# Optimization experiments

Hardware: AMD Instinct MI355X
Metric: run time of the kernel (lower is better)

The kernel has to match this reference:

```python
import jax, jax.numpy as jnp
import numpy as np

DIM = 4096
N_HEADS = 32
N_KV_HEADS = 8
HEAD_DIM = DIM // N_HEADS  # 128
N_REP = N_HEADS // N_KV_HEADS  # 4
SEQ = 2048
BLOCK = 64
N_BLK = SEQ // BLOCK  # 32
TOPK = 8
NEG = -1e30


def _rope(x, cos, sin):
    # x: (B, L, H, D); cos/sin: (L, D/2). Pairs are interleaved (..., D/2, 2)
    B, L, H, D = x.shape
    xr = x.reshape(B, L, H, D // 2, 2)
    x0, x1 = xr[..., 0], xr[..., 1]
    c = cos[None, :, None, :]
    s = sin[None, :, None, :]
    o0 = x0 * c - x1 * s
    o1 = x0 * s + x1 * c
    return jnp.stack([o0, o1], axis=-1).reshape(B, L, H, D)


def setup_inputs() -> dict:
    key = jax.random.key(0)
    ks = jax.random.split(key, 8)
    x = jax.random.normal(ks[0], (1, SEQ, DIM), dtype=jnp.float32)
    # true RoPE angles (theta = 10000^{-2i/D})
    inv_freq = 1.0 / (10000.0 ** (np.arange(0, HEAD_DIM, 2, dtype=np.float32) / HEAD_DIM))
    angles = np.arange(SEQ, dtype=np.float32)[:, None] * inv_freq[None, :]  # (L, D/2)
    cos = jnp.asarray(np.cos(angles))
    sin = jnp.asarray(np.sin(angles))
    sc = 0.02
    wq = jax.random.normal(ks[1], (DIM, N_HEADS * HEAD_DIM), dtype=jnp.float32) * sc
    wk = jax.random.normal(ks[2], (DIM, N_KV_HEADS * HEAD_DIM), dtype=jnp.float32) * sc
    wv = jax.random.normal(ks[3], (DIM, N_KV_HEADS * HEAD_DIM), dtype=jnp.float32) * sc
    wo = jax.random.normal(ks[4], (N_HEADS * HEAD_DIM, DIM), dtype=jnp.float32) * sc
    return {"x": x, "cos": cos, "sin": sin, "wq": wq, "wk": wk, "wv": wv, "wo": wo}


def reference(x, cos, sin, wq, wk, wv, wo):
    B, L, _ = x.shape
    # QKV projections
    q = (x @ wq).reshape(B, L, N_HEADS, HEAD_DIM)
    k = (x @ wk).reshape(B, L, N_KV_HEADS, HEAD_DIM)
    v = (x @ wv).reshape(B, L, N_KV_HEADS, HEAD_DIM)
    # rotary embeddings on q and k
    q = _rope(q, cos, sin)
    k = _rope(k, cos, sin)
    # GQA: expand kv heads n_rep times
    k = jnp.repeat(k, N_REP, axis=2)  # (B, L, Hq, D)
    v = jnp.repeat(v, N_REP, axis=2)
    q = q.transpose(0, 2, 1, 3)  # (B, H, L, D)
    k = k.transpose(0, 2, 1, 3)
    v = v.transpose(0, 2, 1, 3)
    scale = 1.0 / jnp.sqrt(jnp.asarray(HEAD_DIM, dtype=q.dtype))

    pos = jnp.arange(L)
    causal = pos[None, :] <= pos[:, None]  # (Lq, Lk): key <= query

    # Block representatives: mean key per block -> top-k block selection per query
    k_blk = k.reshape(B, N_HEADS, N_BLK, BLOCK, HEAD_DIM).mean(axis=3)  # (B,H,Nblk,D)
    blk_scores = jnp.einsum('bhqd,bhnd->bhqn', q, k_blk) * scale  # (B,H,L,Nblk)
    blk_start = jnp.arange(N_BLK) * BLOCK
    blk_allowed = blk_start[None, :] <= pos[:, None]  # (L, Nblk)
    blk_scores = jnp.where(blk_allowed[None, None], blk_scores, NEG)
    _, top_idx = jax.lax.top_k(blk_scores, TOPK)  # (B,H,L,TOPK)
    blk_mask = jax.nn.one_hot(top_idx, N_BLK, dtype=jnp.bool_).any(axis=-2)  # (B,H,L,Nblk)

    # Expand block mask to per-key mask, combine with causal
    key_mask = jnp.repeat(blk_mask, BLOCK, axis=-1)  # (B,H,L,S)
    key_mask = key_mask & causal[None, None]

    scores = jnp.einsum('bhqd,bhkd->bhqk', q, k) * scale  # (B,H,L,S)
    scores = jnp.where(key_mask, scores, NEG)
    attn = jax.nn.softmax(scores, axis=-1)
    out = jnp.einsum('bhqk,bhkd->bhqd', attn, v)  # (B,H,L,D)
    out = out.transpose(0, 2, 1, 3).reshape(B, L, N_HEADS * HEAD_DIM)
    return out @ wo
```

## Files before the change

kernel.cpp:

```cpp
#include <hip/hip_runtime.h>
#include <hip/hip_bf16.h>
#include <math.h>

#define SEQ 2048
#define DIM 4096
#define NH 32
#define HD 128
#define NKV 8
#define NREP 4
#define BLOCK 64
#define NBLK 32
#define TOPK 8
#define KVDIM (NKV * HD)
#define SCALE 0.08838834764831845f

__device__ inline unsigned short f2b(float f) {
    __hip_bfloat16 h = __float2bfloat16(f);
    return *reinterpret_cast<unsigned short*>(&h);
}
__device__ inline float bitsf(unsigned int u) {
    union { float f; unsigned int i; } x; x.i = u; return x.f;
}
__device__ inline float b2f(unsigned short us) { return bitsf(((unsigned int)us) << 16); }
__device__ inline void unpack2(unsigned int w0, float* o) {
    o[0] = bitsf(w0 << 16);
    o[1] = bitsf(w0 & 0xffff0000u);
}
__device__ inline void unpack4(uint2 w, float* o) { unpack2(w.x, o); unpack2(w.y, o + 2); }
__device__ inline void unpack8(uint4 w, float* o) {
    unpack2(w.x, o); unpack2(w.y, o + 2); unpack2(w.z, o + 4); unpack2(w.w, o + 6);
}
__device__ inline float dot4f(float4 a, float4 b) {
    return a.x * b.x + a.y * b.y + a.z * b.z + a.w * b.w;
}

typedef __attribute__((ext_vector_type(8))) short bfrag;
typedef __attribute__((ext_vector_type(4))) float ffrag;

__device__ __forceinline__ void gl_lds16(const void* g, void* l) {
    __builtin_amdgcn_global_load_lds((const __attribute__((address_space(1))) void*)g,
                                     (__attribute__((address_space(3))) void*)l, 16, 0, 0);
}

template <bool SPLIT>
__global__ __launch_bounds__(256) void mfma_gemm(const unsigned short* __restrict__ Ah,
                                                 const unsigned short* __restrict__ Al,
                                                 const unsigned short* __restrict__ Bh,
                                                 const unsigned short* __restrict__ Bl,
                                                 float* __restrict__ C,
                                                 int M, int N, int K) {
    __shared__ short As[(SPLIT ? 2 : 1) * 4096];
    __shared__ short Bs[(SPLIT ? 2 : 1) * 4096];

    const int tid = threadIdx.x;
    const int lane = tid & 63;
    const int w = tid >> 6;
    const int wm = (w >> 1) * 64;
    const int wn = (w & 1) * 64;
    const int m = lane & 15;
    const int quad = lane >> 4;
    const int bm = blockIdx.y * 128;
    const int bn = blockIdx.x * 128;

    const int r0 = tid >> 2;
    const int c0 = (tid & 3) * 8;
    const size_t aoff0 = (size_t)(bm + r0) * K + c0;
    const size_t aoff1 = (size_t)(bm + r0 + 64) * K + c0;
    const size_t boff0 = (size_t)(bn + r0) * K + c0;
    const size_t boff1 = (size_t)(bn + r0 + 64) * K + c0;

    ffrag acc[4][4];
    const ffrag z = {0.f, 0.f, 0.f, 0.f};
#pragma unroll
    for (int i = 0; i < 4; ++i)
#pragma unroll
        for (int j = 0; j < 4; ++j) acc[i][j] = z;

    for (int kt = 0; kt < K; kt += 32) {
        __syncthreads();
        gl_lds16(Ah + aoff0 + kt, As + tid * 8);
        gl_lds16(Ah + aoff1 + kt, As + 2048 + tid * 8);
        gl_lds16(Bh + boff0 + kt, Bs + tid * 8);
        gl_lds16(Bh + boff1 + kt, Bs + 2048 + tid * 8);
        if constexpr (SPLIT) {
            gl_lds16(Al + aoff0 + kt, As + 4096 + tid * 8);
            gl_lds16(Al + aoff1 + kt, As + 6144 + tid * 8);
            gl_lds16(Bl + boff0 + kt, Bs + 4096 + tid * 8);
            gl_lds16(Bl + boff1 + kt, Bs + 6144 + tid * 8);
        }
        __syncthreads();

        bfrag ah[4], bh[4];
#pragma unroll
        for (int i = 0; i < 4; ++i)
            ah[i] = *(const bfrag*)(As + (wm + i * 16 + m) * 32 + quad * 8);
#pragma unroll
        for (int j = 0; j < 4; ++j)
            bh[j] = *(const bfrag*)(Bs + (wn + j * 16 + m) * 32 + quad * 8);
        if constexpr (SPLIT) {
            bfrag al[4], bl[4];
#pragma unroll
            for (int i = 0; i < 4; ++i)
                al[i] = *(const bfrag*)(As + 4096 + (wm + i * 16 + m) * 32 + quad * 8);
#pragma unroll
            for (int j = 0; j < 4; ++j)
                bl[j] = *(const bfrag*)(Bs + 4096 + (wn + j * 16 + m) * 32 + quad * 8);
#pragma unroll
            for (int i = 0; i < 4; ++i)
#pragma unroll
                for (int j = 0; j < 4; ++j) {
                    acc[i][j] = __builtin_amdgcn_mfma_f32_16x16x32_bf16(ah[i], bh[j], acc[i][j], 0, 0, 0);
                    acc[i][j] = __builtin_amdgcn_mfma_f32_16x16x32_bf16(ah[i], bl[j], acc[i][j], 0, 0, 0);
                    acc[i][j] = __builtin_amdgcn_mfma_f32_16x16x32_bf16(al[i], bh[j], acc[i][j], 0, 0, 0);
                }
        } else {
#pragma unroll
            for (int i = 0; i < 4; ++i)
#pragma unroll
                for (int j = 0; j < 4; ++j)
                    acc[i][j] = __builtin_amdgcn_mfma_f32_16x16x32_bf16(ah[i], bh[j], acc[i][j], 0, 0, 0);
        }
    }

#pragma unroll
    for (int i = 0; i < 4; ++i)
#pragma unroll
        for (int j = 0; j < 4; ++j)
#pragma unroll
            for (int r = 0; r < 4; ++r)
                C[(size_t)(bm + wm + i * 16 + quad * 4 + r) * N + bn + wn + j * 16 + m] =
                    acc[i][j][r];
}

__global__ __launch_bounds__(256) void transpose_conv(const float* __restrict__ W,
                                                      unsigned short* __restrict__ Th,
                                                      unsigned short* __restrict__ Tl,
                                                      int K, int N, int rowoff) {
    __shared__ float tile[32][36];
    const int k0 = blockIdx.y * 32, n0 = blockIdx.x * 32;
    const int t = threadIdx.x;
    const int r = t >> 3, c4 = (t & 7) * 4;
    *(float4*)&tile[r][c4] = *(const float4*)(W + (size_t)(k0 + r) * N + n0 + c4);
    __syncthreads();
    float v0 = tile[c4 + 0][r], v1 = tile[c4 + 1][r], v2 = tile[c4 + 2][r], v3 = tile[c4 + 3][r];
    ushort4 h;
    h.x = f2b(v0); h.y = f2b(v1); h.z = f2b(v2); h.w = f2b(v3);
    const size_t ooff = (size_t)(rowoff + n0 + r) * K + k0 + c4;
    *(ushort4*)(Th + ooff) = h;
    if (Tl) {
        ushort4 l;
        l.x = f2b(v0 - b2f(h.x)); l.y = f2b(v1 - b2f(h.y));
        l.z = f2b(v2 - b2f(h.z)); l.w = f2b(v3 - b2f(h.w));
        *(ushort4*)(Tl + ooff) = l;
    }
}

__global__ void conv_hilo(const float* __restrict__ X, unsigned short* __restrict__ H,
                          unsigned short* __restrict__ L) {
    const int i = (blockIdx.x * blockDim.x + threadIdx.x) * 4;
    const float4 x = *(const float4*)(X + i);
    ushort4 h;
    h.x = f2b(x.x); h.y = f2b(x.y); h.z = f2b(x.z); h.w = f2b(x.w);
    *(ushort4*)(H + i) = h;
    if (L) {
        ushort4 l;
        l.x = f2b(x.x - b2f(h.x)); l.y = f2b(x.y - b2f(h.y));
        l.z = f2b(x.z - b2f(h.z)); l.w = f2b(x.w - b2f(h.w));
        *(ushort4*)(L + i) = l;
    }
}

__global__ void kconv_kernel(const float* __restrict__ kvf, unsigned short* __restrict__ kb) {
    const int i = (blockIdx.x * blockDim.x + threadIdx.x) * 4;
    const int s = i >> 10, c = i & 1023;
    const float4 x = *(const float4*)(kvf + (size_t)s * 2048 + c);
    ushort4 h;
    h.x = f2b(x.x); h.y = f2b(x.y); h.z = f2b(x.z); h.w = f2b(x.w);
    *(ushort4*)(kb + (size_t)s * 1024 + c) = h;
}

__global__ __launch_bounds__(256) void vtrans_kernel(const float* __restrict__ kvf,
                                                     unsigned short* __restrict__ vt) {
    __shared__ unsigned short tile[64][72];
    const int s0 = blockIdx.x * 64;
    const int c0 = blockIdx.y * 64;
    const int t = threadIdx.x;
    const int r = t >> 4;
    const int c4 = (t & 15) * 4;
#pragma unroll
    for (int u = 0; u < 4; ++u) {
        const float4 x = *(const float4*)(kvf + (size_t)(s0 + u * 16 + r) * 2048 + 1024 + c0 + c4);
        ushort4 hh;
        hh.x = f2b(x.x); hh.y = f2b(x.y); hh.z = f2b(x.z); hh.w = f2b(x.w);
        *(ushort4*)(&tile[u * 16 + r][c4]) = hh;
    }
    __syncthreads();
    const int cc = t >> 2;
    const int sg = (t & 3) * 16;
    union { unsigned short s[16]; uint4 v[2]; } bb;
#pragma unroll
    for (int i = 0; i < 16; ++i) bb.s[i] = tile[sg + i][cc];
    unsigned short* op = vt + (size_t)(c0 + cc) * 2048 + s0 + sg;
    *(uint4*)op = bb.v[0];
    *(uint4*)(op + 8) = bb.v[1];
}

__global__ __launch_bounds__(256) void gemm_kernel(const float* __restrict__ A,
                                                   const float* __restrict__ B,
                                                   float* __restrict__ C,
                                                   int M, int N, int K) {
    __shared__ __align__(16) float As[16][68];
    __shared__ __align__(16) float Bs[16][68];

    const int tid = threadIdx.x;
    const int bm = blockIdx.y * 64;
    const int bn = blockIdx.x * 64;
    const int tm = (tid >> 4) * 4;
    const int tn = (tid & 15) * 4;

    float acc[4][4] = {};

    for (int k0 = 0; k0 < K; k0 += 16) {
        {
            const int mm = tid >> 2;
            const int kk = (tid & 3) * 4;
            const float* ap = A + (size_t)(bm + mm) * K + k0 + kk;
            const float4 a4 = *reinterpret_cast<const float4*>(ap);
            As[kk + 0][mm] = a4.x;
            As[kk + 1][mm] = a4.y;
            As[kk + 2][mm] = a4.z;
            As[kk + 3][mm] = a4.w;
        }
        {
            const int kk = tid >> 4;
            const int n = (tid & 15) * 4;
            const float* bp = B + (size_t)(k0 + kk) * N + bn + n;
            *reinterpret_cast<float4*>(&Bs[kk][n]) = *reinterpret_cast<const float4*>(bp);
        }
        __syncthreads();
#pragma unroll
        for (int kk = 0; kk < 16; ++kk) {
            const float4 a4 = *reinterpret_cast<const float4*>(&As[kk][tm]);
            const float4 b4 = *reinterpret_cast<const float4*>(&Bs[kk][tn]);
            const float av[4] = {a4.x, a4.y, a4.z, a4.w};
            const float bv[4] = {b4.x, b4.y, b4.z, b4.w};
#pragma unroll
            for (int i = 0; i < 4; ++i)
#pragma unroll
                for (int j = 0; j < 4; ++j) acc[i][j] += av[i] * bv[j];
        }
        __syncthreads();
    }
#pragma unroll
    for (int i = 0; i < 4; ++i)
#pragma unroll
        for (int j = 0; j < 4; ++j)
            C[(size_t)(bm + tm + i) * N + bn + tn + j] = acc[i][j];
}

__global__ void rope_kernel(float* __restrict__ x, const float* __restrict__ cosb,
                            const float* __restrict__ sinb, int nh, int stride) {
    const int idx = blockIdx.x * blockDim.x + threadIdx.x;
    const int i = idx & 63;
    const int h = (idx >> 6) % nh;
    const int pos = idx / (64 * nh);
    const float c = cosb[pos * 64 + i];
    const float s = sinb[pos * 64 + i];
    float* p = x + (size_t)pos * stride + h * HD + 2 * i;
    const float x0 = p[0], x1 = p[1];
    p[0] = x0 * c - x1 * s;
    p[1] = x0 * s + x1 * c;
}

__global__ void blkmean_kernel(const float* __restrict__ k, float* __restrict__ kblk,
                               int stride) {
    const int idx = blockIdx.x * blockDim.x + threadIdx.x;
    const int d = idx & 127;
    const int blk = (idx >> 7) & 31;
    const int kv = idx >> 12;
    float s = 0.f;
#pragma unroll 8
    for (int r = 0; r < BLOCK; ++r)
        s += k[(size_t)(blk * BLOCK + r) * stride + kv * HD + d];
    kblk[idx] = s * (1.f / 64.f);
}

__global__ __launch_bounds__(256) void attn_mfma_kernel(const float* __restrict__ q,
                                                        const unsigned short* __restrict__ kbp,
                                                        const unsigned short* __restrict__ vtp,
                                                        const float* __restrict__ kblk,
                                                        float* __restrict__ out) {
    __shared__ __align__(16) unsigned char smem[62720];
    unsigned short* qsb = (unsigned short*)smem;
    unsigned short* ksb = (unsigned short*)(smem + 17408);
    unsigned short* vsb = (unsigned short*)(smem + 34816);
    unsigned short* psb = (unsigned short*)(smem + 53248);
    unsigned int*  selm = (unsigned int*)(smem + 62464);
    float* qff = (float*)smem;
    float* kbf = (float*)(smem + 33792);
    float* bsc = (float*)(smem + 50688);

    const int qt = 31 - blockIdx.x;
    const int h = blockIdx.y;
    const int kv = h >> 2;
    const int qbase = qt * 64;
    const int tid = threadIdx.x;
    const int lane = tid & 63;
    const int w = tid >> 6;
    const int m = lane & 15;
    const int quad = lane >> 4;
    const int wm = w * 16;

#pragma unroll
    for (int u = 0; u < 8; ++u) {
        const int idx = u * 1024 + tid * 4;
        const int qi = idx >> 7, d = idx & 127;
        *(float4*)(qff + qi * 132 + d) =
            *(const float4*)(q + ((size_t)((qbase + qi) * NH + h)) * HD + d);
    }
#pragma unroll
    for (int u = 0; u < 4; ++u) {
        const int idx = u * 1024 + tid * 4;
        const int b = idx >> 7, d = idx & 127;
        *(float4*)(kbf + b * 132 + d) =
            *(const float4*)(kblk + ((size_t)(kv * NBLK + b)) * HD + d);
    }
    __syncthreads();

    {
        float acc[4][2] = {};
#pragma unroll 4
        for (int d = 0; d < 128; d += 4) {
            float4 qv[4], kb2[2];
#pragma unroll
            for (int i = 0; i < 4; ++i) qv[i] = *(float4*)(qff + (quad + 4 * w + 16 * i) * 132 + d);
#pragma unroll
            for (int j = 0; j < 2; ++j) kb2[j] = *(float4*)(kbf + (m + 16 * j) * 132 + d);
#pragma unroll
            for (int i = 0; i < 4; ++i)
#pragma unroll
                for (int j = 0; j < 2; ++j) acc[i][j] += dot4f(qv[i], kb2[j]);
        }
#pragma unroll
        for (int i = 0; i < 4; ++i)
#pragma unroll
            for (int j = 0; j < 2; ++j) {
                const int b = m + 16 * j;
                if (b <= qt) bsc[(quad + 4 * w + 16 * i) * 33 + b] = acc[i][j];
            }
    }
    __syncthreads();

    if (tid < 64) {
        const int ns = (qt + 1 < TOPK) ? qt + 1 : TOPK;
        unsigned int sel = 0;
        const float* br = bsc + tid * 33;
        for (int t2 = 0; t2 < ns; ++t2) {
            float best = -3.4e38f; int bi = 0;
            for (int b = 0; b <= qt; ++b)
                if (!((sel >> b) & 1u) && br[b] > best) { best = br[b]; bi = b; }
            sel |= 1u << bi;
        }
        selm[tid] = sel;
    }
    __syncthreads();

    unsigned int uni = 0;
    {
        float tmp[32];
#pragma unroll
        for (int u = 0; u < 8; ++u) {
            const int idx = u * 1024 + tid * 4;
            *(float4*)(tmp + u * 4) = *(float4*)(qff + (idx >> 7) * 132 + (idx & 127));
        }
        for (int i = 0; i < 64; ++i) uni |= selm[i];
        __syncthreads();
#pragma unroll
        for (int u = 0; u < 8; ++u) {
            const int idx = u * 1024 + tid * 4;
            const int qi = idx >> 7, d = idx & 127;
            ushort4 qu;
            qu.x = f2b(tmp[u * 4 + 0]); qu.y = f2b(tmp[u * 4 + 1]);
            qu.z = f2b(tmp[u * 4 + 2]); qu.w = f2b(tmp[u * 4 + 3]);
            *(ushort4*)(qsb + qi * 136 + d) = qu;
        }
    }

    unsigned int selr[4];
#pragma unroll
    for (int r = 0; r < 4; ++r) selr[r] = selm[wm + quad * 4 + r];

    float m_run[4], l_run[4];
#pragma unroll
    for (int r = 0; r < 4; ++r) { m_run[r] = -3.0e38f; l_run[r] = 0.f; }
    ffrag o[8];
    const ffrag z = {0.f, 0.f, 0.f, 0.f};
#pragma unroll
    for (int n = 0; n < 8; ++n) o[n] = z;

    unsigned short* psw = psb + w * (16 * 72);

    for (int b = 0; b <= qt; ++b) {
        if (!((uni >> b) & 1u)) continue;
        __syncthreads();
#pragma unroll
        for (int u = 0; u < 4; ++u) {
            const int idx = u * 256 + tid;
            const int r = idx >> 4, dseg = (idx & 15) * 8;
            *(uint4*)(ksb + r * 136 + dseg) =
                *(const uint4*)(kbp + (size_t)(b * 64 + r) * 1024 + kv * 128 + dseg);
        }
#pragma unroll
        for (int u = 0; u < 4; ++u) {
            const int idx = u * 256 + tid;
            const int d = idx >> 3, ks8 = (idx & 7) * 8;
            *(uint4*)(vsb + d * 72 + ks8) =
                *(const uint4*)(vtp + (size_t)(kv * 128 + d) * 2048 + b * 64 + ks8);
        }
        __syncthreads();

        ffrag s[4];
#pragma unroll
        for (int j = 0; j < 4; ++j) s[j] = z;
#pragma unroll
        for (int ks = 0; ks < 4; ++ks) {
            const bfrag aq = *(const bfrag*)(qsb + (wm + m) * 136 + ks * 32 + quad * 8);
#pragma unroll
            for (int j = 0; j < 4; ++j) {
                const bfrag bk = *(const bfrag*)(ksb + (j * 16 + m) * 136 + ks * 32 + quad * 8);
                s[j] = __builtin_amdgcn_mfma_f32_16x16x32_bf16(aq, bk, s[j], 0, 0, 0);
            }
        }

        const bool diag = (b == qt);
        float a_r[4];
#pragma unroll
        for (int r = 0; r < 4; ++r) {
            const int rloc = quad * 4 + r;
            const int rtile = wm + rloc;
            const bool selb = (selr[r] >> b) & 1u;
            float sv[4];
#pragma unroll
            for (int j = 0; j < 4; ++j) {
                const int col = j * 16 + m;
                const bool valid = selb && (!diag || col <= rtile);
                sv[j] = valid ? s[j][r] * SCALE : -3.0e38f;
            }
            float t = fmaxf(fmaxf(sv[0], sv[1]), fmaxf(sv[2], sv[3]));
            t = fmaxf(t, __shfl_xor(t, 1));
            t = fmaxf(t, __shfl_xor(t, 2));
            t = fmaxf(t, __shfl_xor(t, 4));
            t = fmaxf(t, __shfl_xor(t, 8));
            const float mo = m_run[r];
            const float mn = fmaxf(mo, t);
            a_r[r] = __expf(mo - mn);
            float sum = 0.f;
#pragma unroll
            for (int j = 0; j < 4; ++j) {
                const float p = (sv[j] > -1.0e30f) ? __expf(sv[j] - mn) : 0.f;
                psw[rloc * 72 + j * 16 + m] = f2b(p);
                sum += p;
            }
            sum += __shfl_xor(sum, 1);
            sum += __shfl_xor(sum, 2);
            sum += __shfl_xor(sum, 4);
            sum += __shfl_xor(sum, 8);
            l_run[r] = l_run[r] * a_r[r] + sum;
            m_run[r] = mn;
        }
#pragma unroll
        for (int n = 0; n < 8; ++n)
#pragma unroll
            for (int r = 0; r < 4; ++r) o[n][r] *= a_r[r];

#pragma unroll
        for (int ks = 0; ks < 2; ++ks) {
            const bfrag pa = *(const bfrag*)(psw + m * 72 + ks * 32 + quad * 8);
#pragma unroll
            for (int n = 0; n < 8; ++n) {
                const bfrag bv = *(const bfrag*)(vsb + (n * 16 + m) * 72 + ks * 32 + quad * 8);
                o[n] = __builtin_amdgcn_mfma_f32_16x16x32_bf16(pa, bv, o[n], 0, 0, 0);
            }
        }
    }

#pragma unroll
    for (int r = 0; r < 4; ++r) {
        const float inv = 1.f / l_run[r];
        float* op = out + ((size_t)((qbase + wm + quad * 4 + r) * NH + h)) * HD + m;
#pragma unroll
        for (int n = 0; n < 8; ++n) op[n * 16] = o[n][r] * inv;
    }
}

__global__ __launch_bounds__(256) void attn_tile_kernel(const float* __restrict__ q,
                                                        const float* __restrict__ kptr,
                                                        const float* __restrict__ vptr,
                                                        const float* __restrict__ kblk,
                                                        float* __restrict__ out,
                                                        int kvstride) {
    __shared__ __align__(16) unsigned char smem[62464];
    unsigned short* ksb = (unsigned short*)smem;
    unsigned short* vsb = (unsigned short*)(smem + 17408);
    unsigned short* psb = (unsigned short*)(smem + 34816);
    unsigned short* qsb = (unsigned short*)(smem + 43520);
    float* mrow = (float*)(smem + 60928);
    float* lrow = (float*)(smem + 61184);
    float* arow = (float*)(smem + 61440);
    float* mnew = (float*)(smem + 61696);
    unsigned int* selm = (unsigned int*)(smem + 61952);
    float* qf  = (float*)smem;
    float* kbf = (float*)(smem + 33792);
    float* bsc = (float*)(smem + 50688);

    const int qt = 31 - blockIdx.x;
    const int h = blockIdx.y;
    const int kv = h >> 2;
    const int qbase = qt * 64;
    const int tid = threadIdx.x;
    const int lane = tid & 63;
    const int w = tid >> 6;
    const int kl = lane & 15;
    const int ql = lane >> 4;

#pragma unroll
    for (int u = 0; u < 8; ++u) {
        const int idx = u * 1024 + tid * 4;
        const int qi = idx >> 7, d = idx & 127;
        *(float4*)(qf + qi * 132 + d) =
            *(const float4*)(q + ((size_t)((qbase + qi) * NH + h)) * HD + d);
    }
#pragma unroll
    for (int u = 0; u < 4; ++u) {
        const int idx = u * 1024 + tid * 4;
        const int b = idx >> 7, d = idx & 127;
        *(float4*)(kbf + b * 132 + d) =
            *(const float4*)(kblk + ((size_t)(kv * NBLK + b)) * HD + d);
    }
    __syncthreads();

    {
        float acc[4][2] = {};
#pragma unroll 4
        for (int d = 0; d < 128; d += 4) {
            float4 qv[4], kb2[2];
#pragma unroll
            for (int i = 0; i < 4; ++i) qv[i] = *(float4*)(qf + (ql + 4 * w + 16 * i) * 132 + d);
#pragma unroll
            for (int j = 0; j < 2; ++j) kb2[j] = *(float4*)(kbf + (kl + 16 * j) * 132 + d);
#pragma unroll
            for (int i = 0; i < 4; ++i)
#pragma unroll
                for (int j = 0; j < 2; ++j) acc[i][j] += dot4f(qv[i], kb2[j]);
        }
#pragma unroll
        for (int i = 0; i < 4; ++i)
#pragma unroll
            for (int j = 0; j < 2; ++j) {
                const int b = kl + 16 * j;
                if (b <= qt) bsc[(ql + 4 * w + 16 * i) * 33 + b] = acc[i][j];
            }
    }
    __syncthreads();

    if (tid < 64) {
        const int ns = (qt + 1 < TOPK) ? qt + 1 : TOPK;
        unsigned int sel = 0;
        const float* br = bsc + tid * 33;
        for (int t = 0; t < ns; ++t) {
            float best = -3.4e38f; int bi = 0;
            for (int b = 0; b <= qt; ++b)
                if (!((sel >> b) & 1u) && br[b] > best) { best = br[b]; bi = b; }
            sel |= 1u << bi;
        }
        selm[tid] = sel;
        mrow[tid] = -3.0e38f;
        lrow[tid] = 0.f;
    }
    __syncthreads();

    unsigned int uni = 0;
    {
        float tmp[32];
#pragma unroll
        for (int u = 0; u < 8; ++u) {
            const int idx = u * 1024 + tid * 4;
            *(float4*)(tmp + u * 4) = *(float4*)(qf + (idx >> 7) * 132 + (idx & 127));
        }
        for (int i = 0; i < 64; ++i) uni |= selm[i];
#pragma unroll
        for (int u = 0; u < 8; ++u) {
            const int idx = u * 1024 + tid * 4;
            const int qi = idx >> 7, d = idx & 127;
            ushort4 qu;
            qu.x = f2b(tmp[u * 4 + 0]); qu.y = f2b(tmp[u * 4 + 1]);
            qu.z = f2b(tmp[u * 4 + 2]); qu.w = f2b(tmp[u * 4 + 3]);
            *(ushort4*)(qsb + qi * 136 + d) = qu;
        }
    }
    __syncthreads();

    const int qi_r[4] = {ql + 4 * w, ql + 4 * w + 16, ql + 4 * w + 32, ql + 4 * w + 48};
    unsigned int selq[4];
#pragma unroll
    for (int i = 0; i < 4; ++i) selq[i] = selm[qi_r[i]];

    float O[4][8] = {};

    for (int b = 0; b <= qt; ++b) {
        if (!((uni >> b) & 1u)) continue;
        __syncthreads();
#pragma unroll
        for (int u = 0; u < 8; ++u) {
            const int idx = u * 1024 + tid * 4;
            const int r = idx >> 7, d = idx & 127;
            const size_t gof = (size_t)(b * 64 + r) * kvstride + kv * HD + d;
            const float4 k4 = *(const float4*)(kptr + gof);
            const float4 v4 = *(const float4*)(vptr + gof);
            ushort4 ku, vu;
            ku.x = f2b(k4.x); ku.y = f2b(k4.y); ku.z = f2b(k4.z); ku.w = f2b(k4.w);
            vu.x = f2b(v4.x); vu.y = f2b(v4.y); vu.z = f2b(v4.z); vu.w = f2b(v4.w);
            *(ushort4*)(ksb + r * 136 + d) = ku;
            *(ushort4*)(vsb + r * 136 + d) = vu;
        }
        __syncthreads();

        float S[4][4] = {};
#pragma unroll 4
        for (int d = 0; d < 128; d += 4) {
            float qv[4][4], kk4[4][4];
#pragma unroll
            for (int i = 0; i < 4; ++i) unpack4(*(uint2*)(qsb + qi_r[i] * 136 + d), qv[i]);
#pragma unroll
            for (int j = 0; j < 4; ++j) unpack4(*(uint2*)(ksb + (kl + 16 * j) * 136 + d), kk4[j]);
#pragma unroll
            for (int i = 0; i < 4; ++i)
#pragma unroll
                for (int j = 0; j < 4; ++j)
#pragma unroll
                    for (int e = 0; e < 4; ++e) S[i][j] += qv[i][e] * kk4[j][e];
        }

        const bool diag = (b == qt);
        float tm[4];
#pragma unroll
        for (int i = 0; i < 4; ++i) {
            const bool selb = (selq[i] >> b) & 1u;
#pragma unroll
            for (int j = 0; j < 4; ++j) {
                const int kj = kl + 16 * j;
                const bool valid = selb && (!diag || kj <= qi_r[i]);
                S[i][j] = valid ? S[i][j] * SCALE : -3.0e38f;
            }
            float t = fmaxf(fmaxf(S[i][0], S[i][1]), fmaxf(S[i][2], S[i][3]));
            t = fmaxf(t, __shfl_xor(t, 1));
            t = fmaxf(t, __shfl_xor(t, 2));
            t = fmaxf(t, __shfl_xor(t, 4));
            t = fmaxf(t, __shfl_xor(t, 8));
            tm[i] = t;
        }
        if (kl == 0) {
#pragma unroll
            for (int i = 0; i < 4; ++i) {
                const float mo = mrow[qi_r[i]];
                const float mn = fmaxf(mo, tm[i]);
                mrow[qi_r[i]] = mn;
                mnew[qi_r[i]] = mn;
                arow[qi_r[i]] = __expf(mo - mn);
            }
        }
        __syncthreads();

        float tl[4];
#pragma unroll
        for (int i = 0; i < 4; ++i) {
            const float mn = mnew[qi_r[i]];
            float sum = 0.f;
#pragma unroll
            for (int j = 0; j < 4; ++j) {
                const float p = (S[i][j] > -1.0e30f) ? __expf(S[i][j] - mn) : 0.f;
                psb[qi_r[i] * 68 + kl + 16 * j] = f2b(p);
                sum += p;
            }
            sum += __shfl_xor(sum, 1);
            sum += __shfl_xor(sum, 2);
            sum += __shfl_xor(sum, 4);
            sum += __shfl_xor(sum, 8);
            tl[i] = sum;
        }
        if (kl == 0) {
#pragma unroll
            for (int i = 0; i < 4; ++i)
                lrow[qi_r[i]] = lrow[qi_r[i]] * arow[qi_r[i]] + tl[i];
        }
#pragma unroll
        for (int i = 0; i < 4; ++i) {
            const float a = arow[qi_r[i]];
#pragma unroll
            for (int e = 0; e < 8; ++e) O[i][e] *= a;
        }
        __syncthreads();

#pragma unroll 4
        for (int kj = 0; kj < 64; ++kj) {
            float p[4];
#pragma unroll
            for (int i = 0; i < 4; ++i) {
                unsigned short us = psb[qi_r[i] * 68 + kj];
                p[i] = bitsf(((unsigned int)us) << 16);
            }
            float vv[8];
            unpack8(*(uint4*)(vsb + kj * 136 + kl * 8), vv);
#pragma unroll
            for (int i = 0; i < 4; ++i)
#pragma unroll
                for (int e = 0; e < 8; ++e) O[i][e] += p[i] * vv[e];
        }
    }
    __syncthreads();

#pragma unroll
    for (int i = 0; i < 4; ++i) {
        const float inv = 1.f / lrow[qi_r[i]];
        float4 o0, o1;
        o0.x = O[i][0] * inv; o0.y = O[i][1] * inv; o0.z = O[i][2] * inv; o0.w = O[i][3] * inv;
        o1.x = O[i][4] * inv; o1.y = O[i][5] * inv; o1.z = O[i][6] * inv; o1.w = O[i][7] * inv;
        float* op = out + ((size_t)((qbase + qi_r[i]) * NH + h)) * HD + kl * 8;
        *(float4*)op = o0;
        *(float4*)(op + 4) = o1;
    }
}

extern "C" void kernel_launch(void* const* d_in, const int* in_sizes, int n_in,
                              void* d_out, int out_size, void* d_ws, size_t ws_size,
                              hipStream_t stream) {
    const float* x    = (const float*)d_in[0];
    const float* cosb = (const float*)d_in[1];
    const float* sinb = (const float*)d_in[2];
    const float* wq   = (const float*)d_in[3];
    const float* wk   = (const float*)d_in[4];
    const float* wv   = (const float*)d_in[5];
    const float* wo   = (const float*)d_in[6];

    unsigned char* ws = (unsigned char*)d_ws;
    const dim3 t256(256);

    const size_t MAIN_REQ = 184680448ull;
    if (ws_size >= MAIN_REQ) {
        float*          qf     = (float*)(ws);
        float*          kvf    = (float*)(ws + 33554432ull);
        float*          kblk   = (float*)(ws + 50331648ull);
        unsigned short* x_hi   = (unsigned short*)(ws + 50462720ull);
        unsigned short* x_lo   = (unsigned short*)(ws + 67239936ull);
        float*          attn   = (float*)(ws + 50462720ull);
        unsigned short* wqT_hi = (unsigned short*)(ws + 84017152ull);
        unsigned short* wqT_lo = (unsigned short*)(ws + 117571584ull);
        unsigned short* kvT_hi = (unsigned short*)(ws + 151126016ull);
        unsigned short* kvT_lo = (unsigned short*)(ws + 167903232ull);
        unsigned short* woT_hi = wqT_hi;
        unsigned short* attnbf = wqT_lo;
        unsigned short* kb16   = kvT_hi;
        unsigned short* vtb    = kvT_lo;

        conv_hilo<<<SEQ * DIM / 4 / 256, t256, 0, stream>>>(x, x_hi, x_lo);
        transpose_conv<<<dim3(DIM / 32, DIM / 32), t256, 0, stream>>>(wq, wqT_hi, wqT_lo, DIM, DIM, 0);
        transpose_conv<<<dim3(KVDIM / 32, DIM / 32), t256, 0, stream>>>(wk, kvT_hi, kvT_lo, DIM, KVDIM, 0);
        transpose_conv<<<dim3(KVDIM / 32, DIM / 32), t256, 0, stream>>>(wv, kvT_hi, kvT_lo, DIM, KVDIM, KVDIM);

        hipLaunchKernelGGL((mfma_gemm<true>), dim3(DIM / 128, SEQ / 128), t256, 0, stream,
                           x_hi, x_lo, wqT_hi, wqT_lo, qf, SEQ, DIM, DIM);
        hipLaunchKernelGGL((mfma_gemm<true>), dim3(2 * KVDIM / 128, SEQ / 128), t256, 0, stream,
                           x_hi, x_lo, kvT_hi, kvT_lo, kvf, SEQ, 2 * KVDIM, DIM);
        transpose_conv<<<dim3(DIM / 32, DIM / 32), t256, 0, stream>>>(wo, woT_hi, nullptr, DIM, DIM, 0);

        rope_kernel<<<(SEQ * NH * 64) / 256, t256, 0, stream>>>(qf, cosb, sinb, NH, NH * HD);
        rope_kernel<<<(SEQ * NKV * 64) / 256, t256, 0, stream>>>(kvf, cosb, sinb, NKV, 2 * KVDIM);
        blkmean_kernel<<<(NKV * NBLK * HD) / 256, t256, 0, stream>>>(kvf, kblk, 2 * KVDIM);

        kconv_kernel<<<(SEQ * KVDIM / 4) / 256, t256, 0, stream>>>(kvf, kb16);
        vtrans_kernel<<<dim3(SEQ / 64, KVDIM / 64), t256, 0, stream>>>(kvf, vtb);

        attn_mfma_kernel<<<dim3(NBLK, NH), t256, 0, stream>>>(qf, kb16, vtb, kblk, attn);

        conv_hilo<<<SEQ * DIM / 4 / 256, t256, 0, stream>>>(attn, attnbf, nullptr);
        hipLaunchKernelGGL((mfma_gemm<false>), dim3(DIM / 128, SEQ / 128), t256, 0, stream,
                           attnbf, nullptr, woT_hi, nullptr, (float*)d_out, SEQ, DIM, DIM);
    } else {
        float* qf   = (float*)ws;
        float* kf   = qf + (size_t)SEQ * DIM;
        float* vf   = kf + (size_t)SEQ * KVDIM;
        float* kblk = vf + (size_t)SEQ * KVDIM;
        float* attn = kblk + (size_t)NKV * NBLK * HD;

        gemm_kernel<<<dim3(DIM / 64, SEQ / 64), t256, 0, stream>>>(x, wq, qf, SEQ, DIM, DIM);
        gemm_kernel<<<dim3(KVDIM / 64, SEQ / 64), t256, 0, stream>>>(x, wk, kf, SEQ, KVDIM, DIM);
        gemm_kernel<<<dim3(KVDIM / 64, SEQ / 64), t256, 0, stream>>>(x, wv, vf, SEQ, KVDIM, DIM);
        rope_kernel<<<(SEQ * NH * 64) / 256, t256, 0, stream>>>(qf, cosb, sinb, NH, NH * HD);
        rope_kernel<<<(SEQ * NKV * 64) / 256, t256, 0, stream>>>(kf, cosb, sinb, NKV, KVDIM);
        blkmean_kernel<<<(NKV * NBLK * HD) / 256, t256, 0, stream>>>(kf, kblk, KVDIM);
        attn_tile_kernel<<<dim3(NBLK, NH), t256, 0, stream>>>(qf, kf, vf, kblk, attn, KVDIM);
        gemm_kernel<<<dim3(DIM / 64, SEQ / 64), t256, 0, stream>>>(attn, wo, (float*)d_out, SEQ, DIM, DIM);
    }
}
```

Before: 940.8 us.

## Prefetch K/V tiles into registers, keep Q in registers, skip top-k for early tiles

The attention kernel now keeps the Q fragments in registers as bf16 and no longer stages Q in shared memory. This shrinks LDS use so three workgroups can fit per CU. It iterates only over the selected blocks via ctz and prefetches the next K/V tile into registers while the current one is computed. Block scoring and top-k are skipped when the query tile has at most TOPK causal blocks, since all of them are selected anyway. It also adds MFMA priority hints and an XCD-aware workgroup swizzle in both the GEMM and the attention kernel. The cost is higher register pressure from the prefetch buffers.

```diff
diff --git a/kernel.cpp b/kernel.cpp
--- a/kernel.cpp
+++ b/kernel.cpp
@@ -59,8 +59,20 @@
     const int wn = (w & 1) * 64;
     const int m = lane & 15;
     const int quad = lane >> 4;
-    const int bm = blockIdx.y * 128;
-    const int bn = blockIdx.x * 128;
+
+    int bx = blockIdx.x, by = blockIdx.y;
+    {
+        const int nwg = gridDim.x * gridDim.y;
+        if ((nwg & 7) == 0) {
+            const int flat = by * gridDim.x + bx;
+            const int nper = nwg >> 3;
+            const int swz = (flat & 7) * nper + (flat >> 3);
+            bx = swz % gridDim.x;
+            by = swz / gridDim.x;
+        }
+    }
+    const int bm = by * 128;
+    const int bn = bx * 128;
 
     const int r0 = tid >> 2;
     const int c0 = (tid & 3) * 8;
@@ -285,23 +297,28 @@
     kblk[idx] = s * (1.f / 64.f);
 }
 
-__global__ __launch_bounds__(256) void attn_mfma_kernel(const float* __restrict__ q,
-                                                        const unsigned short* __restrict__ kbp,
-                                                        const unsigned short* __restrict__ vtp,
-                                                        const float* __restrict__ kblk,
-                                                        float* __restrict__ out) {
-    __shared__ __align__(16) unsigned char smem[62720];
-    unsigned short* qsb = (unsigned short*)smem;
-    unsigned short* ksb = (unsigned short*)(smem + 17408);
-    unsigned short* vsb = (unsigned short*)(smem + 34816);
-    unsigned short* psb = (unsigned short*)(smem + 53248);
-    unsigned int*  selm = (unsigned int*)(smem + 62464);
-    float* qff = (float*)smem;
-    float* kbf = (float*)(smem + 33792);
-    float* bsc = (float*)(smem + 50688);
-
-    const int qt = 31 - blockIdx.x;
-    const int h = blockIdx.y;
+__global__ __launch_bounds__(256, 3) void attn_mfma_kernel(const float* __restrict__ q,
+                                                           const unsigned short* __restrict__ kbp,
+                                                           const unsigned short* __restrict__ vtp,
+                                                           const float* __restrict__ kblk,
+                                                           float* __restrict__ out) {
+    __shared__ __align__(16) unsigned char smem[45568];
+    unsigned short* ksb = (unsigned short*)smem;
+    unsigned short* vsb = (unsigned short*)(smem + 17408);
+    unsigned short* psb = (unsigned short*)(smem + 35840);
+    unsigned int*  selm = (unsigned int*)(smem + 45056);
+    float* kbf = (float*)smem;
+    float* bsc = (float*)(smem + 16896);
+
+    int bx = blockIdx.x, by = blockIdx.y;
+    {
+        const int flat = by * 32 + bx;
+        const int swz = (flat & 7) * 128 + (flat >> 3);
+        bx = swz & 31;
+        by = swz >> 5;
+    }
+    const int qt = 31 - bx;
+    const int h = by;
     const int kv = h >> 2;
     const int qbase = qt * 64;
     const int tid = threadIdx.x;
@@ -311,84 +328,80 @@
     const int quad = lane >> 4;
     const int wm = w * 16;
 
-#pragma unroll
-    for (int u = 0; u < 8; ++u) {
-        const int idx = u * 1024 + tid * 4;
-        const int qi = idx >> 7, d = idx & 127;
-        *(float4*)(qff + qi * 132 + d) =
-            *(const float4*)(q + ((size_t)((qbase + qi) * NH + h)) * HD + d);
-    }
-#pragma unroll
-    for (int u = 0; u < 4; ++u) {
-        const int idx = u * 1024 + tid * 4;
-        const int b = idx >> 7, d = idx & 127;
-        *(float4*)(kbf + b * 132 + d) =
-            *(const float4*)(kblk + ((size_t)(kv * NBLK + b)) * HD + d);
-    }
-    __syncthreads();
-
+    unsigned int uni;
+    if (qt + 1 > TOPK) {
+#pragma unroll
+        for (int u = 0; u < 4; ++u) {
+            const int idx = u * 1024 + tid * 4;
+            const int b = idx >> 7, d = idx & 127;
+            *(float4*)(kbf + b * 132 + d) =
+                *(const float4*)(kblk + ((size_t)(kv * NBLK + b)) * HD + d);
+        }
+        __syncthreads();
+        {
+            float acc[4][2] = {};
+            const int r0 = quad + 4 * w;
+#pragma unroll 4
+            for (int d = 0; d < 128; d += 4) {
+                float4 qv[4], kb2[2];
+#pragma unroll
+                for (int i = 0; i < 4; ++i)
+                    qv[i] = *(const float4*)(q + ((size_t)((qbase + r0 + 16 * i) * NH + h)) * HD + d);
+#pragma unroll
+                for (int j = 0; j < 2; ++j) kb2[j] = *(float4*)(kbf + (m + 16 * j) * 132 + d);
+#pragma unroll
+                for (int i = 0; i < 4; ++i)
+#pragma unroll
+                    for (int j = 0; j < 2; ++j) acc[i][j] += dot4f(qv[i], kb2[j]);
+            }
+#pragma unroll
+            for (int i = 0; i < 4; ++i)
+#pragma unroll
+                for (int j = 0; j < 2; ++j) {
+                    const int b = m + 16 * j;
+                    if (b <= qt) bsc[(r0 + 16 * i) * 33 + b] = acc[i][j];
+                }
+        }
+        __syncthreads();
+        if (tid < 64) {
+            unsigned int sel = 0;
+            const float* br = bsc + tid * 33;
+            for (int t2 = 0; t2 < TOPK; ++t2) {
+                float best = -3.4e38f; int bi = 0;
+                for (int b = 0; b <= qt; ++b)
+                    if (!((sel >> b) & 1u) && br[b] > best) { best = br[b]; bi = b; }
+                sel |= 1u << bi;
+            }
+            selm[tid] = sel;
+        }
+        __syncthreads();
+        unsigned int u2 = 0;
+        for (int i = 0; i < 64; ++i) u2 |= selm[i];
+        uni = u2;
+    } else {
+        uni = (2u << qt) - 1;
+    }
+
+    unsigned int selr[4];
+#pragma unroll
+    for (int r = 0; r < 4; ++r)
+        selr[r] = (qt + 1 > TOPK) ? selm[wm + quad * 4 + r] : uni;
+
+    bfrag aq[4];
     {
-        float acc[4][2] = {};
-#pragma unroll 4
-        for (int d = 0; d < 128; d += 4) {
-            float4 qv[4], kb2[2];
-#pragma unroll
-            for (int i = 0; i < 4; ++i) qv[i] = *(float4*)(qff + (quad + 4 * w + 16 * i) * 132 + d);
-#pragma unroll
-            for (int j = 0; j < 2; ++j) kb2[j] = *(float4*)(kbf + (m + 16 * j) * 132 + d);
-#pragma unroll
-            for (int i = 0; i < 4; ++i)
-#pragma unroll
-                for (int j = 0; j < 2; ++j) acc[i][j] += dot4f(qv[i], kb2[j]);
-        }
-#pragma unroll
-        for (int i = 0; i < 4; ++i)
-#pragma unroll
-            for (int j = 0; j < 2; ++j) {
-                const int b = m + 16 * j;
-                if (b <= qt) bsc[(quad + 4 * w + 16 * i) * 33 + b] = acc[i][j];
-            }
-    }
-    __syncthreads();
-
-    if (tid < 64) {
-        const int ns = (qt + 1 < TOPK) ? qt + 1 : TOPK;
-        unsigned int sel = 0;
-        const float* br = bsc + tid * 33;
-        for (int t2 = 0; t2 < ns; ++t2) {
-            float best = -3.4e38f; int bi = 0;
-            for (int b = 0; b <= qt; ++b)
-                if (!((sel >> b) & 1u) && br[b] > best) { best = br[b]; bi = b; }
-            sel |= 1u << bi;
-        }
-        selm[tid] = sel;
-    }
-    __syncthreads();
-
-    unsigned int uni = 0;
-    {
-        float tmp[32];
-#pragma unroll
-        for (int u = 0; u < 8; ++u) {
-            const int idx = u * 1024 + tid * 4;
-            *(float4*)(tmp + u * 4) = *(float4*)(qff + (idx >> 7) * 132 + (idx & 127));
-        }
-        for (int i = 0; i < 64; ++i) uni |= selm[i];
-        __syncthreads();
-#pragma unroll
-        for (int u = 0; u < 8; ++u) {
-            const int idx = u * 1024 + tid * 4;
-            const int qi = idx >> 7, d = idx & 127;
-            ushort4 qu;
-            qu.x = f2b(tmp[u * 4 + 0]); qu.y = f2b(tmp[u * 4 + 1]);
-            qu.z = f2b(tmp[u * 4 + 2]); qu.w = f2b(tmp[u * 4 + 3]);
-            *(ushort4*)(qsb + qi * 136 + d) = qu;
-        }
-    }
-
-    unsigned int selr[4];
-#pragma unroll
-    for (int r = 0; r < 4; ++r) selr[r] = selm[wm + quad * 4 + r];
+        const float* qrow = q + ((size_t)((qbase + wm + m) * NH + h)) * HD;
+#pragma unroll
+        for (int ks = 0; ks < 4; ++ks) {
+            const float4 f0 = *(const float4*)(qrow + ks * 32 + quad * 8);
+            const float4 f1 = *(const float4*)(qrow + ks * 32 + quad * 8 + 4);
+            bfrag a;
+            a[0] = (short)f2b(f0.x); a[1] = (short)f2b(f0.y);
+            a[2] = (short)f2b(f0.z); a[3] = (short)f2b(f0.w);
+            a[4] = (short)f2b(f1.x); a[5] = (short)f2b(f1.y);
+            a[6] = (short)f2b(f1.z); a[7] = (short)f2b(f1.w);
+            aq[ks] = a;
+        }
+    }
 
     float m_run[4], l_run[4];
 #pragma unroll
@@ -400,37 +413,65 @@
 
     unsigned short* psw = psb + w * (16 * 72);
 
-    for (int b = 0; b <= qt; ++b) {
-        if (!((uni >> b) & 1u)) continue;
-        __syncthreads();
+    uint4 kreg[4], vreg[4];
+    unsigned int rem = uni;
+    if (rem) {
+        const int b0 = __builtin_ctz(rem);
 #pragma unroll
         for (int u = 0; u < 4; ++u) {
             const int idx = u * 256 + tid;
-            const int r = idx >> 4, dseg = (idx & 15) * 8;
-            *(uint4*)(ksb + r * 136 + dseg) =
-                *(const uint4*)(kbp + (size_t)(b * 64 + r) * 1024 + kv * 128 + dseg);
+            kreg[u] = *(const uint4*)(kbp + (size_t)(b0 * 64 + (idx >> 4)) * 1024 + kv * 128 + (idx & 15) * 8);
         }
 #pragma unroll
         for (int u = 0; u < 4; ++u) {
             const int idx = u * 256 + tid;
-            const int d = idx >> 3, ks8 = (idx & 7) * 8;
-            *(uint4*)(vsb + d * 72 + ks8) =
-                *(const uint4*)(vtp + (size_t)(kv * 128 + d) * 2048 + b * 64 + ks8);
-        }
-        __syncthreads();
+            vreg[u] = *(const uint4*)(vtp + (size_t)(kv * 128 + (idx >> 3)) * 2048 + b0 * 64 + (idx & 7) * 8);
+        }
+    }
+
+    while (rem) {
+        const int b = __builtin_ctz(rem);
+        rem &= rem - 1;
+        __syncthreads();
+#pragma unroll
+        for (int u = 0; u < 4; ++u) {
+            const int idx = u * 256 + tid;
+            *(uint4*)(ksb + (idx >> 4) * 136 + (idx & 15) * 8) = kreg[u];
+        }
+#pragma unroll
+        for (int u = 0; u < 4; ++u) {
+            const int idx = u * 256 + tid;
+            *(uint4*)(vsb + (idx >> 3) * 72 + (idx & 7) * 8) = vreg[u];
+        }
+        const bool hn = (rem != 0);
+        const int bn = hn ? __builtin_ctz(rem) : 0;
+        __syncthreads();
+        if (hn) {
+#pragma unroll
+            for (int u = 0; u < 4; ++u) {
+                const int idx = u * 256 + tid;
+                kreg[u] = *(const uint4*)(kbp + (size_t)(bn * 64 + (idx >> 4)) * 1024 + kv * 128 + (idx & 15) * 8);
+            }
+#pragma unroll
+            for (int u = 0; u < 4; ++u) {
+                const int idx = u * 256 + tid;
+                vreg[u] = *(const uint4*)(vtp + (size_t)(kv * 128 + (idx >> 3)) * 2048 + bn * 64 + (idx & 7) * 8);
+            }
+        }
 
         ffrag s[4];
 #pragma unroll
         for (int j = 0; j < 4; ++j) s[j] = z;
+        __builtin_amdgcn_s_setprio(1);
 #pragma unroll
         for (int ks = 0; ks < 4; ++ks) {
-            const bfrag aq = *(const bfrag*)(qsb + (wm + m) * 136 + ks * 32 + quad * 8);
 #pragma unroll
             for (int j = 0; j < 4; ++j) {
                 const bfrag bk = *(const bfrag*)(ksb + (j * 16 + m) * 136 + ks * 32 + quad * 8);
-                s[j] = __builtin_amdgcn_mfma_f32_16x16x32_bf16(aq, bk, s[j], 0, 0, 0);
-            }
-        }
+                s[j] = __builtin_amdgcn_mfma_f32_16x16x32_bf16(aq[ks], bk, s[j], 0, 0, 0);
+            }
+        }
+        __builtin_amdgcn_s_setprio(0);
 
         const bool diag = (b == qt);
         float a_r[4];
@@ -473,6 +514,7 @@
 #pragma unroll
             for (int r = 0; r < 4; ++r) o[n][r] *= a_r[r];
 
+        __builtin_amdgcn_s_setprio(1);
 #pragma unroll
         for (int ks = 0; ks < 2; ++ks) {
             const bfrag pa = *(const bfrag*)(psw + m * 72 + ks * 32 + quad * 8);
@@ -482,6 +524,7 @@
                 o[n] = __builtin_amdgcn_mfma_f32_16x16x32_bf16(pa, bv, o[n], 0, 0, 0);
             }
         }
+        __builtin_amdgcn_s_setprio(0);
     }
 
 #pragma unroll
```

Result: slower. 979.8 us (+4.2%).
